# Kernel tuning notes

Hardware: AMD Instinct MI355X
Metric: run time of the kernel (lower is better)

## Reference

```python
import jax, jax.numpy as jnp
import numpy as np

B, S, D = 2, 2048, 1024
H, HD, R = 16, 64, 128
BLOCK, TOPK = 64, 4
ROPE_BASE = 100000.0
NEG = -1e30  # finite large-negative instead of -inf to avoid NaN rows


def _rope_tables(seq_len, dim, dtype):
    inv_freq = 1.0 / (ROPE_BASE ** (jnp.arange(0, dim, 2, dtype=jnp.float32) / dim))
    freqs = jnp.arange(seq_len, dtype=jnp.float32)[:, None] * inv_freq[None, :]  # [S, dim/2]
    emb = jnp.concatenate([freqs, freqs], axis=-1)  # [S, dim]
    return jnp.cos(emb).astype(dtype), jnp.sin(emb).astype(dtype)


def _rotate_half(t):
    t1, t2 = jnp.split(t, 2, axis=-1)
    return jnp.concatenate([-t2, t1], axis=-1)


def _apply_rope(t, cos, sin):
    # t: [B, H, S, HD]; cos/sin: [S, HD]
    return t * cos[None, None] + _rotate_half(t) * sin[None, None]


def setup_inputs() -> dict:
    key = jax.random.key(0)
    ks = jax.random.split(key, 6)
    s = 0.02
    return {
        "x": jax.random.normal(ks[0], (B, S, D), jnp.float32),
        "w_q": jax.random.normal(ks[1], (D, D), jnp.float32) * s,
        "w_kv_down": jax.random.normal(ks[2], (R, D), jnp.float32) * s,
        "w_kv_up": jax.random.normal(ks[3], (2 * D, R), jnp.float32) * s,
        "w_out": jax.random.normal(ks[4], (D, D), jnp.float32) * s,
        "w_scorer": jax.random.normal(ks[5], (1, D), jnp.float32) * s,
    }


def reference(x, w_q, w_kv_down, w_kv_up, w_out, w_scorer):
    b, s, d = x.shape
    nb = s // BLOCK  # S divisible by block_size here

    q = (x @ w_q.T).reshape(b, s, H, HD).transpose(0, 2, 1, 3)  # [B,H,S,HD]
    latent = x @ w_kv_down.T                                      # [B,S,R]
    kv = latent @ w_kv_up.T                                       # [B,S,2D]
    k, v = jnp.split(kv, 2, axis=-1)
    k = k.reshape(b, s, H, HD).transpose(0, 2, 1, 3)
    v = v.reshape(b, s, H, HD).transpose(0, 2, 1, 3)

    cos, sin = _rope_tables(s, HD, x.dtype)
    q = _apply_rope(q, cos, sin)
    k = _apply_rope(k, cos, sin)

    # block relevance scores from mean-pooled block reps of x
    block_reps = x.reshape(b, nb, BLOCK, d).mean(axis=2)          # [B,nb,D]
    block_scores = (block_reps @ w_scorer.T)[..., 0]              # [B,nb]
    _, top_idx = jax.lax.top_k(block_scores, min(TOPK, nb))       # [B,topk]

    # sparse key mask: True where key position lies in a selected block
    sel = jnp.zeros((b, nb), dtype=bool)
    sel = sel.at[jnp.arange(b)[:, None], top_idx].set(True)       # [B,nb]
    sparse_mask = jnp.repeat(sel, BLOCK, axis=1)                  # [B,S]

    causal = jnp.tril(jnp.ones((s, s), dtype=bool))               # True = allowed
    allowed = sparse_mask[:, None, None, :] & causal[None, None]  # [B,1,S,S]

    scale = 1.0 / jnp.sqrt(jnp.asarray(HD, x.dtype))
    scores = jnp.einsum("bhqd,bhkd->bhqk", q, k) * scale          # [B,H,S,S]
    scores = jnp.where(allowed, scores, NEG)
    attn = jax.nn.softmax(scores, axis=-1)
    out = jnp.einsum("bhqk,bhkd->bhqd", attn, v)                  # [B,H,S,HD]
    out = out.transpose(0, 2, 1, 3).reshape(b, s, d)
    return out @ w_out.T
```

## Files before the change

kernel.cpp:

```cpp
#include <hip/hip_runtime.h>
#include <hip/hip_bf16.h>
#include <math.h>

#define B_ 2
#define S_ 2048
#define D_ 1024
#define H_ 16
#define HD_ 64
#define R_ 128
#define NBLK 32
#define TOPK_ 4
#define BS_ (B_*S_)

typedef __attribute__((ext_vector_type(8))) short bf16x8;
typedef __attribute__((ext_vector_type(4))) float f32x4;

__device__ __forceinline__ unsigned short f2bf(float f) {
    unsigned int u = __float_as_uint(f);
    u += 0x7fffu + ((u >> 16) & 1u);
    return (unsigned short)(u >> 16);
}
__device__ __forceinline__ float bf2f(unsigned short h) {
    return __uint_as_float(((unsigned int)h) << 16);
}
__device__ __forceinline__ unsigned int pack2(float a, float b) {
    return (unsigned int)f2bf(a) | ((unsigned int)f2bf(b) << 16);
}
__device__ __forceinline__ void gload_lds16(const void* g, void* l) {
    __builtin_amdgcn_global_load_lds((const __attribute__((address_space(1))) void*)g,
                                     (__attribute__((address_space(3))) void*)l, 16, 0, 0);
}

__global__ void rope_tables_k(float* __restrict__ cosT, float* __restrict__ sinT) {
    int idx = blockIdx.x*256 + threadIdx.x;
    if (idx >= S_*HD_) return;
    int s  = idx >> 6;
    int hd = idx & 63;
    int j = (hd < 32) ? hd : hd - 32;
    float inv = powf(100000.0f, -((float)(2*j) / 64.0f));
    float fr = (float)s * inv;
    cosT[idx] = cosf(fr);
    sinT[idx] = sinf(fr);
}

__global__ __launch_bounds__(256) void cvtw_k(const float* __restrict__ wq,
        const float* __restrict__ wkd, const float* __restrict__ wku,
        const float* __restrict__ wo, unsigned short* __restrict__ wcat,
        unsigned short* __restrict__ wkub, unsigned short* __restrict__ wob) {
    const int blk = blockIdx.x;
    const float* src; unsigned short* dst; int base;
    if      (blk < 512) { src = wq;  dst = wcat;            base = blk;       }
    else if (blk < 576) { src = wkd; dst = wcat + 1048576;  base = blk - 512; }
    else if (blk < 704) { src = wku; dst = wkub;            base = blk - 576; }
    else                { src = wo;  dst = wob;             base = blk - 704; }
    const int i = base*2048 + threadIdx.x*8;
    float4 a = *(const float4*)&src[i];
    float4 b = *(const float4*)&src[i+4];
    uint4 o;
    o.x = pack2(a.x, a.y); o.y = pack2(a.z, a.w);
    o.z = pack2(b.x, b.y); o.w = pack2(b.z, b.w);
    *(uint4*)&dst[i] = o;
}

template<int EPI>
__global__ __launch_bounds__(256) void gemm_mfma_k(const unsigned short* __restrict__ A,
        const unsigned short* __restrict__ Bm, int M, int N, int K,
        void* __restrict__ o0, void* __restrict__ o1,
        const float* __restrict__ cosT, const float* __restrict__ sinT) {
    __shared__ unsigned short As[128*64];
    __shared__ unsigned short Bs[64*64];
    const int tid  = threadIdx.x;
    const int wave = tid >> 6, lane = tid & 63;
    const int bm = blockIdx.y << 7, bn = blockIdx.x << 6;
    const int g  = lane >> 4, qc = lane & 15;
    const int srow  = lane >> 3;
    const int sslot = (lane & 7) ^ srow;

    f32x4 acc[2][4];
    #pragma unroll
    for (int m=0;m<2;m++)
        #pragma unroll
        for (int n=0;n<4;n++)
            acc[m][n] = (f32x4){0.f,0.f,0.f,0.f};

    for (int k0 = 0; k0 < K; k0 += 64) {
        __syncthreads();
        #pragma unroll
        for (int it = 0; it < 4; ++it) {
            const int chunk = (it << 2) | wave;
            const int row   = (chunk << 3) | srow;
            gload_lds16(A + (size_t)(bm + row) * K + k0 + (sslot << 3), &As[chunk << 9]);
        }
        #pragma unroll
        for (int it = 0; it < 2; ++it) {
            const int chunk = (it << 2) | wave;
            const int row   = (chunk << 3) | srow;
            gload_lds16(Bm + (size_t)(bn + row) * K + k0 + (sslot << 3), &Bs[chunk << 9]);
        }
        __syncthreads();
        #pragma unroll
        for (int ks = 0; ks < 2; ++ks) {
            const int swb = ((ks << 2) | g) ^ (lane & 7);
            bf16x8 af[2], bfr[4];
            #pragma unroll
            for (int m = 0; m < 2; ++m)
                af[m]  = *(const bf16x8*)&As[(((wave << 5) + (m << 4) + qc) << 6) + (swb << 3)];
            #pragma unroll
            for (int n = 0; n < 4; ++n)
                bfr[n] = *(const bf16x8*)&Bs[(((n << 4) + qc) << 6) + (swb << 3)];
            #pragma unroll
            for (int m = 0; m < 2; ++m)
                #pragma unroll
                for (int n = 0; n < 4; ++n)
                    acc[m][n] = __builtin_amdgcn_mfma_f32_16x16x32_bf16(af[m], bfr[n], acc[m][n], 0, 0, 0);
        }
    }

    if (EPI == 0) {
        float* C = (float*)o0;
        #pragma unroll
        for (int m = 0; m < 2; ++m) {
            const int r0 = bm + (wave << 5) + (m << 4) + (g << 2);
            #pragma unroll
            for (int n = 0; n < 4; ++n) {
                const int c = bn + (n << 4) + qc;
                #pragma unroll
                for (int j = 0; j < 4; ++j)
                    C[(size_t)(r0 + j) * N + c] = acc[m][n][j];
            }
        }
    } else {
        const bool isrope = (bn < 1024);
        if (isrope) {
            const int h = bn >> 6;
            unsigned short* dst = (unsigned short*)o0;
            #pragma unroll
            for (int m = 0; m < 2; ++m) {
                const int r0 = bm + (wave << 5) + (m << 4) + (g << 2);
                #pragma unroll
                for (int j = 0; j < 4; ++j) {
                    const int row = r0 + j;
                    const int b = row >> 11, s = row & (S_-1);
                    const size_t obase = ((size_t)(b*H_ + h) * S_ + s) << 6;
                    #pragma unroll
                    for (int n = 0; n < 4; ++n) {
                        const int hd = (n << 4) + qc;
                        const float c_ = cosT[(s << 6) + hd];
                        const float sn = sinT[(s << 6) + hd];
                        const float rot = (n < 2) ? -acc[m][n ^ 2][j] : acc[m][n ^ 2][j];
                        dst[obase + hd] = f2bf(acc[m][n][j] * c_ + rot * sn);
                    }
                }
            }
        } else if (EPI == 1) {
            unsigned short* latb = (unsigned short*)o1;
            const int c0 = bn - 1024;
            #pragma unroll
            for (int m = 0; m < 2; ++m) {
                const int r0 = bm + (wave << 5) + (m << 4) + (g << 2);
                #pragma unroll
                for (int n = 0; n < 4; ++n) {
                    const int c = c0 + (n << 4) + qc;
                    #pragma unroll
                    for (int j = 0; j < 4; ++j)
                        latb[(size_t)(r0 + j) * R_ + c] = f2bf(acc[m][n][j]);
                }
            }
        } else {
            const int h = (bn >> 6) - 16;
            unsigned short* vrb = (unsigned short*)o1;
            #pragma unroll
            for (int m = 0; m < 2; ++m) {
                const int r0 = bm + (wave << 5) + (m << 4) + (g << 2);
                #pragma unroll
                for (int j = 0; j < 4; ++j) {
                    const int row = r0 + j;
                    const int b = row >> 11, s = row & (S_-1);
                    const size_t obase = ((size_t)(b*H_ + h) * S_ + s) << 6;
                    #pragma unroll
                    for (int n = 0; n < 4; ++n)
                        vrb[obase + (n << 4) + qc] = f2bf(acc[m][n][j]);
                }
            }
        }
    }
}

__global__ __launch_bounds__(256) void rowscore_cvt_k(const float* __restrict__ x,
        const float* __restrict__ wsc, float* __restrict__ rows,
        unsigned short* __restrict__ xb) {
    const int wid  = (blockIdx.x << 2) + (threadIdx.x >> 6);
    const int lane = threadIdx.x & 63;
    #pragma unroll
    for (int r = 0; r < 4; ++r) {
        const int row = (wid << 2) + r;
        const float* xp = x + (size_t)row * D_;
        unsigned short* xo = xb + (size_t)row * D_;
        float acc = 0.f;
        #pragma unroll
        for (int j = 0; j < 4; ++j) {
            const int off = ((j << 6) + lane) << 2;
            float4 xv = *(const float4*)&xp[off];
            float4 wv = *(const float4*)&wsc[off];
            acc = fmaf(xv.x, wv.x, acc);
            acc = fmaf(xv.y, wv.y, acc);
            acc = fmaf(xv.z, wv.z, acc);
            acc = fmaf(xv.w, wv.w, acc);
            uint2 o; o.x = pack2(xv.x, xv.y); o.y = pack2(xv.z, xv.w);
            *(uint2*)&xo[off] = o;
        }
        #pragma unroll
        for (int m = 1; m <= 32; m <<= 1) acc += __shfl_xor(acc, m);
        if (lane == 0) rows[row] = acc;
    }
}

__global__ __launch_bounds__(256) void blocktopk_k(const float* __restrict__ rows,
        int* __restrict__ sel) {
    __shared__ float bs[64];
    const int bk = threadIdx.x >> 2, qt = threadIdx.x & 3;
    const float* rp = rows + (bk << 6) + (qt << 4);
    float p = 0.f;
    #pragma unroll
    for (int i = 0; i < 16; ++i) p += rp[i];
    p += __shfl_xor(p, 1);
    p += __shfl_xor(p, 2);
    if (qt == 0) bs[bk] = p;
    __syncthreads();
    if (threadIdx.x < B_) {
        const int b = threadIdx.x;
        float sc[NBLK];
        for (int i = 0; i < NBLK; ++i) sc[i] = bs[b * NBLK + i];
        for (int j = 0; j < TOPK_; ++j) {
            float best = -INFINITY; int bi = 0;
            for (int i = 0; i < NBLK; ++i)
                if (sc[i] > best) { best = sc[i]; bi = i; }
            sel[b * TOPK_ + j] = bi;
            sc[bi] = -INFINITY;
        }
    }
}

__global__ __launch_bounds__(256) void vt_k(const unsigned short* __restrict__ vrb,
        unsigned short* __restrict__ vtb, float* __restrict__ vsum) {
    const int wg = blockIdx.x;
    const int bh = wg >> 5;
    __shared__ unsigned short T[64][72];
    const uint4* src = (const uint4*)(vrb + (size_t)wg*4096);
    #pragma unroll
    for (int u=0;u<2;u++) {
        int idx = (u<<8) + threadIdx.x;
        int r = idx>>3, c = (idx&7)<<3;
        *(uint4*)&T[r][c] = src[idx];
    }
    __syncthreads();
    unsigned short* dst = vtb + (size_t)wg*4096;
    #pragma unroll
    for (int u=0;u<2;u++) {
        int idx = (u<<8) + threadIdx.x;
        int dd = idx>>3, k0 = (idx&7)<<3;
        unsigned short tmp[8];
        float sm = 0.f;
        #pragma unroll
        for (int j=0;j<8;j++) { tmp[j] = T[k0+j][dd]; sm += bf2f(tmp[j]); }
        *(uint4*)&dst[(size_t)idx<<3] = *(uint4*)tmp;
        sm += __shfl_xor(sm, 1);
        sm += __shfl_xor(sm, 2);
        sm += __shfl_xor(sm, 4);
        if ((threadIdx.x & 7) == 0) atomicAdd(&vsum[(bh<<6)+dd], sm);
    }
}

__global__ __launch_bounds__(256) void attn_mfma_k(const unsigned short* __restrict__ qrb,
        const unsigned short* __restrict__ krb, const unsigned short* __restrict__ vtb,
        const int* __restrict__ sel, const float* __restrict__ vsum,
        unsigned short* __restrict__ attno) {
    const int qb = blockIdx.x & (NBLK-1);
    const int bh = blockIdx.x >> 5;
    const int b  = bh >> 4;
    const int h  = bh & 15;
    const int tid  = threadIdx.x;
    const int wave = tid >> 6, lane = tid & 63;
    const int g = lane >> 4, qc = lane & 15;

    __shared__ unsigned short Ks[64][72];
    __shared__ unsigned short Vt[64][72];
    __shared__ unsigned short Pl[4][16][72];
    __shared__ float cfl[4][16];
    __shared__ float lvl[4][16];

    int selb[4];
    #pragma unroll
    for (int j=0;j<4;j++) selb[j] = sel[(b<<2)+j];
    const bool diag = (selb[0]==qb)|(selb[1]==qb)|(selb[2]==qb)|(selb[3]==qb);

    const unsigned short* qp = qrb + (((size_t)bh*S_ + (qb<<6) + (wave<<4) + qc) << 6);
    bf16x8 bq[2];
    bq[0] = *(const bf16x8*)(qp + (g<<3));
    bq[1] = *(const bf16x8*)(qp + 32 + (g<<3));

    f32x4 oacc[4];
    #pragma unroll
    for (int n=0;n<4;n++) oacc[n] = (f32x4){0.f,0.f,0.f,0.f};
    float mrun = -INFINITY, lrun = 0.f;
    int nproc = 0;
    const int qib = (wave<<4) + qc;

    for (int j = 0; j < 5; ++j) {
        int kb; bool isdiag;
        if (j < 4) { kb = selb[j]; isdiag = false; if (kb >= qb) continue; }
        else       { if (!diag) continue; kb = qb; isdiag = true; }
        nproc++;
        const uint4* gk = (const uint4*)(krb + (((size_t)bh*S_ + (kb<<6)) << 6));
        const uint4* gv = (const uint4*)(vtb + (((size_t)(bh*NBLK + kb)) << 12));
        __syncthreads();
        #pragma unroll
        for (int u=0;u<2;u++) {
            int idx = (u<<8) + tid;
            int r = idx>>3, c = (idx&7)<<3;
            *(uint4*)&Ks[r][c] = gk[idx];
            *(uint4*)&Vt[r][c] = gv[idx];
        }
        __syncthreads();

        f32x4 sf[4];
        #pragma unroll
        for (int m=0;m<4;m++) sf[m] = (f32x4){0.f,0.f,0.f,0.f};
        #pragma unroll
        for (int ks=0;ks<2;ks++)
            #pragma unroll
            for (int m=0;m<4;m++) {
                bf16x8 ak = *(const bf16x8*)&Ks[(m<<4)+qc][(ks<<5)+(g<<3)];
                sf[m] = __builtin_amdgcn_mfma_f32_16x16x32_bf16(ak, bq[ks], sf[m], 0, 0, 0);
            }

        float s[16];
        float bmax = -INFINITY;
        #pragma unroll
        for (int m=0;m<4;m++)
            #pragma unroll
            for (int r2=0;r2<4;r2++) {
                const int kl = (m<<4)+(g<<2)+r2;
                float v = sf[m][r2]*0.125f;
                if (isdiag && kl > qib) v = -1e30f;
                s[(m<<2)+r2] = v;
                bmax = fmaxf(bmax, v);
            }
        bmax = fmaxf(bmax, __shfl_xor(bmax, 16));
        bmax = fmaxf(bmax, __shfl_xor(bmax, 32));
        const float mnew = fmaxf(mrun, bmax);
        const float cf = __expf(mrun - mnew);
        float ls = 0.f;
        #pragma unroll
        for (int m=0;m<4;m++) {
            float p0 = __expf(s[(m<<2)+0]-mnew);
            float p1 = __expf(s[(m<<2)+1]-mnew);
            float p2 = __expf(s[(m<<2)+2]-mnew);
            float p3 = __expf(s[(m<<2)+3]-mnew);
            ls += p0+p1+p2+p3;
            const int koff = (m<<4)+(g<<2);
            *(unsigned int*)&Pl[wave][qc][koff]   = pack2(p0,p1);
            *(unsigned int*)&Pl[wave][qc][koff+2] = pack2(p2,p3);
        }
        ls += __shfl_xor(ls, 16);
        ls += __shfl_xor(ls, 32);
        lrun = lrun*cf + ls;
        cfl[wave][qc] = cf;
        f32x4 cf4 = *(const f32x4*)&cfl[wave][g<<2];
        #pragma unroll
        for (int n=0;n<4;n++) oacc[n] *= cf4;
        #pragma unroll
        for (int ks=0;ks<2;ks++) {
            bf16x8 pa = *(const bf16x8*)&Pl[wave][qc][(ks<<5)+(g<<3)];
            #pragma unroll
            for (int n=0;n<4;n++) {
                bf16x8 vb = *(const bf16x8*)&Vt[(n<<4)+qc][(ks<<5)+(g<<3)];
                oacc[n] = __builtin_amdgcn_mfma_f32_16x16x32_bf16(pa, vb, oacc[n], 0, 0, 0);
            }
        }
        mrun = mnew;
    }

    f32x4 il4 = (f32x4){0.f,0.f,0.f,0.f};
    if (nproc) {
        lvl[wave][qc] = 1.0f / lrun;
        il4 = *(const f32x4*)&lvl[wave][g<<2];
    }
    #pragma unroll
    for (int n=0;n<4;n++)
        #pragma unroll
        for (int r2=0;r2<4;r2++) {
            float val = nproc ? oacc[n][r2]*il4[r2]
                              : vsum[(bh<<6)+(n<<4)+qc] * (1.0f/(float)S_);
            const int row = (qb<<6) + (wave<<4) + (g<<2) + r2;
            attno[(((size_t)(b*S_+row))<<10) + (h<<6) + (n<<4) + qc] = f2bf(val);
        }
}

extern "C" void kernel_launch(void* const* d_in, const int* in_sizes, int n_in,
                              void* d_out, int out_size, void* d_ws, size_t ws_size,
                              hipStream_t stream) {
    (void)in_sizes; (void)n_in; (void)out_size; (void)ws_size;
    const float* x     = (const float*)d_in[0];
    const float* w_q   = (const float*)d_in[1];
    const float* w_kvd = (const float*)d_in[2];
    const float* w_kvu = (const float*)d_in[3];
    const float* w_o   = (const float*)d_in[4];
    const float* w_sc  = (const float*)d_in[5];
    float* out = (float*)d_out;

    char* p = (char*)d_ws;
    auto alloc = [&](size_t bytes) -> void* {
        void* r = (void*)p;
        p += (bytes + 255) & ~(size_t)255;
        return r;
    };
    float* cosT  = (float*)alloc((size_t)S_*HD_*4);
    float* sinT  = (float*)alloc((size_t)S_*HD_*4);
    unsigned short* xb    = (unsigned short*)alloc((size_t)BS_*D_*2);
    unsigned short* wcat  = (unsigned short*)alloc((size_t)(D_+R_)*D_*2);
    unsigned short* wkub  = (unsigned short*)alloc((size_t)2*D_*R_*2);
    unsigned short* wob   = (unsigned short*)alloc((size_t)D_*D_*2);
    unsigned short* latb  = (unsigned short*)alloc((size_t)BS_*R_*2);
    unsigned short* qrb   = (unsigned short*)alloc((size_t)BS_*D_*2);
    unsigned short* krb   = (unsigned short*)alloc((size_t)BS_*D_*2);
    unsigned short* vrb   = (unsigned short*)alloc((size_t)BS_*D_*2);
    unsigned short* vtb   = (unsigned short*)alloc((size_t)BS_*D_*2);
    unsigned short* attnob= (unsigned short*)alloc((size_t)BS_*D_*2);
    float* rows   = (float*)alloc((size_t)BS_*4);
    int*   sel    = (int*)  alloc((size_t)B_*TOPK_*4);
    float* vsum   = (float*)alloc((size_t)B_*H_*HD_*4);

    rope_tables_k<<<(S_*HD_+255)/256, 256, 0, stream>>>(cosT, sinT);
    cvtw_k<<<1216, 256, 0, stream>>>(w_q, w_kvd, w_kvu, w_o, wcat, wkub, wob);
    rowscore_cvt_k<<<256, 256, 0, stream>>>(x, w_sc, rows, xb);
    blocktopk_k<<<1, 256, 0, stream>>>(rows, sel);

    gemm_mfma_k<1><<<dim3((D_+R_)/64, BS_/128), 256, 0, stream>>>(
        xb, wcat, BS_, D_+R_, D_, qrb, latb, cosT, sinT);
    gemm_mfma_k<2><<<dim3(2*D_/64, BS_/128), 256, 0, stream>>>(
        latb, wkub, BS_, 2*D_, R_, krb, vrb, cosT, sinT);

    hipMemsetAsync(vsum, 0, (size_t)B_*H_*HD_*4, stream);
    vt_k<<<B_*H_*NBLK, 256, 0, stream>>>(vrb, vtb, vsum);
    attn_mfma_k<<<B_*H_*NBLK, 256, 0, stream>>>(qrb, krb, vtb, sel, vsum, attnob);
    gemm_mfma_k<0><<<dim3(D_/64, BS_/128), 256, 0, stream>>>(
        attnob, wob, BS_, D_, D_, out, nullptr, nullptr, nullptr);
}
```

Measured before the change: 160.2 us.

## Fuse V transpose and column sums into KV-up GEMM epilogue; load K/V fragments directly

The separate vt_k kernel is removed. The KV-up GEMM epilogue now stages each V tile in shared memory, writes it out transposed per 64-key block, and atomically accumulates the per-head V column sums. This removes one launch and a full round trip of the intermediate V buffer through global memory. Separately, the attention kernel drops its shared-memory K/V staging and the two barriers per block, loading MFMA fragments straight from global memory into registers. That trades LDS traffic and synchronisation for uncoalesced global loads and higher register pressure.

```diff
diff --git a/kernel.cpp b/kernel.cpp
--- a/kernel.cpp
+++ b/kernel.cpp
@@ -66,9 +66,11 @@
 __global__ __launch_bounds__(256) void gemm_mfma_k(const unsigned short* __restrict__ A,
         const unsigned short* __restrict__ Bm, int M, int N, int K,
         void* __restrict__ o0, void* __restrict__ o1,
-        const float* __restrict__ cosT, const float* __restrict__ sinT) {
-    __shared__ unsigned short As[128*64];
-    __shared__ unsigned short Bs[64*64];
+        const float* __restrict__ cosT, const float* __restrict__ sinT,
+        float* __restrict__ vsum) {
+    __shared__ unsigned short shbuf[128*64 + 64*64];
+    unsigned short* As = shbuf;
+    unsigned short* Bs = shbuf + 128*64;
     const int tid  = threadIdx.x;
     const int wave = tid >> 6, lane = tid & 63;
     const int bm = blockIdx.y << 7, bn = blockIdx.x << 6;
@@ -167,19 +169,39 @@
                 }
             }
         } else {
-            const int h = (bn >> 6) - 16;
-            unsigned short* vrb = (unsigned short*)o1;
+            const int h  = (bn >> 6) - 16;
+            const int b  = bm >> 11, s0 = bm & (S_-1);
+            const int bh = (b << 4) + h;
+            unsigned short* vtb = (unsigned short*)o1;
+            unsigned short (*T)[72] = (unsigned short(*)[72])shbuf;
+            __syncthreads();
             #pragma unroll
             for (int m = 0; m < 2; ++m) {
-                const int r0 = bm + (wave << 5) + (m << 4) + (g << 2);
-                #pragma unroll
-                for (int j = 0; j < 4; ++j) {
-                    const int row = r0 + j;
-                    const int b = row >> 11, s = row & (S_-1);
-                    const size_t obase = ((size_t)(b*H_ + h) * S_ + s) << 6;
+                const int r0 = (wave << 5) + (m << 4) + (g << 2);
+                #pragma unroll
+                for (int n = 0; n < 4; ++n)
                     #pragma unroll
-                    for (int n = 0; n < 4; ++n)
-                        vrb[obase + (n << 4) + qc] = f2bf(acc[m][n][j]);
+                    for (int j = 0; j < 4; ++j)
+                        T[r0 + j][(n << 4) + qc] = f2bf(acc[m][n][j]);
+            }
+            __syncthreads();
+            #pragma unroll
+            for (int u = 0; u < 2; ++u) {
+                const int kb = (s0 >> 6) + u;
+                unsigned short* dst = vtb + (((size_t)(bh * NBLK + kb)) << 12);
+                #pragma unroll
+                for (int uu = 0; uu < 2; ++uu) {
+                    const int idx = (uu << 8) + tid;
+                    const int dd = idx >> 3, k0 = (idx & 7) << 3;
+                    unsigned short tmp[8];
+                    float sm = 0.f;
+                    #pragma unroll
+                    for (int j = 0; j < 8; ++j) { tmp[j] = T[(u << 6) + k0 + j][dd]; sm += bf2f(tmp[j]); }
+                    *(uint4*)&dst[(size_t)(dd << 6) + k0] = *(uint4*)tmp;
+                    sm += __shfl_xor(sm, 1);
+                    sm += __shfl_xor(sm, 2);
+                    sm += __shfl_xor(sm, 4);
+                    if ((tid & 7) == 0) atomicAdd(&vsum[(bh << 6) + dd], sm);
                 }
             }
         }
@@ -241,36 +263,6 @@
     }
 }
 
-__global__ __launch_bounds__(256) void vt_k(const unsigned short* __restrict__ vrb,
-        unsigned short* __restrict__ vtb, float* __restrict__ vsum) {
-    const int wg = blockIdx.x;
-    const int bh = wg >> 5;
-    __shared__ unsigned short T[64][72];
-    const uint4* src = (const uint4*)(vrb + (size_t)wg*4096);
-    #pragma unroll
-    for (int u=0;u<2;u++) {
-        int idx = (u<<8) + threadIdx.x;
-        int r = idx>>3, c = (idx&7)<<3;
-        *(uint4*)&T[r][c] = src[idx];
-    }
-    __syncthreads();
-    unsigned short* dst = vtb + (size_t)wg*4096;
-    #pragma unroll
-    for (int u=0;u<2;u++) {
-        int idx = (u<<8) + threadIdx.x;
-        int dd = idx>>3, k0 = (idx&7)<<3;
-        unsigned short tmp[8];
-        float sm = 0.f;
-        #pragma unroll
-        for (int j=0;j<8;j++) { tmp[j] = T[k0+j][dd]; sm += bf2f(tmp[j]); }
-        *(uint4*)&dst[(size_t)idx<<3] = *(uint4*)tmp;
-        sm += __shfl_xor(sm, 1);
-        sm += __shfl_xor(sm, 2);
-        sm += __shfl_xor(sm, 4);
-        if ((threadIdx.x & 7) == 0) atomicAdd(&vsum[(bh<<6)+dd], sm);
-    }
-}
-
 __global__ __launch_bounds__(256) void attn_mfma_k(const unsigned short* __restrict__ qrb,
         const unsigned short* __restrict__ krb, const unsigned short* __restrict__ vtb,
         const int* __restrict__ sel, const float* __restrict__ vsum,
@@ -283,8 +275,6 @@
     const int wave = tid >> 6, lane = tid & 63;
     const int g = lane >> 4, qc = lane & 15;
 
-    __shared__ unsigned short Ks[64][72];
-    __shared__ unsigned short Vt[64][72];
     __shared__ unsigned short Pl[4][16][72];
     __shared__ float cfl[4][16];
     __shared__ float lvl[4][16];
@@ -311,17 +301,20 @@
         if (j < 4) { kb = selb[j]; isdiag = false; if (kb >= qb) continue; }
         else       { if (!diag) continue; kb = qb; isdiag = true; }
         nproc++;
-        const uint4* gk = (const uint4*)(krb + (((size_t)bh*S_ + (kb<<6)) << 6));
-        const uint4* gv = (const uint4*)(vtb + (((size_t)(bh*NBLK + kb)) << 12));
-        __syncthreads();
-        #pragma unroll
-        for (int u=0;u<2;u++) {
-            int idx = (u<<8) + tid;
-            int r = idx>>3, c = (idx&7)<<3;
-            *(uint4*)&Ks[r][c] = gk[idx];
-            *(uint4*)&Vt[r][c] = gv[idx];
-        }
-        __syncthreads();
+        const unsigned short* kB = krb + (((size_t)bh*S_ + (kb<<6)) << 6);
+        const unsigned short* vT = vtb + (((size_t)(bh*NBLK + kb)) << 12);
+
+        bf16x8 ak[2][4], vb[2][4];
+        #pragma unroll
+        for (int ks=0;ks<2;ks++)
+            #pragma unroll
+            for (int m=0;m<4;m++)
+                ak[ks][m] = *(const bf16x8*)(kB + (((m<<4)+qc)<<6) + (ks<<5) + (g<<3));
+        #pragma unroll
+        for (int ks=0;ks<2;ks++)
+            #pragma unroll
+            for (int n=0;n<4;n++)
+                vb[ks][n] = *(const bf16x8*)(vT + (((n<<4)+qc)<<6) + (ks<<5) + (g<<3));
 
         f32x4 sf[4];
         #pragma unroll
@@ -329,10 +322,8 @@
         #pragma unroll
         for (int ks=0;ks<2;ks++)
             #pragma unroll
-            for (int m=0;m<4;m++) {
-                bf16x8 ak = *(const bf16x8*)&Ks[(m<<4)+qc][(ks<<5)+(g<<3)];
-                sf[m] = __builtin_amdgcn_mfma_f32_16x16x32_bf16(ak, bq[ks], sf[m], 0, 0, 0);
-            }
+            for (int m=0;m<4;m++)
+                sf[m] = __builtin_amdgcn_mfma_f32_16x16x32_bf16(ak[ks][m], bq[ks], sf[m], 0, 0, 0);
 
         float s[16];
         float bmax = -INFINITY;
@@ -373,10 +364,8 @@
         for (int ks=0;ks<2;ks++) {
             bf16x8 pa = *(const bf16x8*)&Pl[wave][qc][(ks<<5)+(g<<3)];
             #pragma unroll
-            for (int n=0;n<4;n++) {
-                bf16x8 vb = *(const bf16x8*)&Vt[(n<<4)+qc][(ks<<5)+(g<<3)];
-                oacc[n] = __builtin_amdgcn_mfma_f32_16x16x32_bf16(pa, vb, oacc[n], 0, 0, 0);
-            }
+            for (int n=0;n<4;n++)
+                oacc[n] = __builtin_amdgcn_mfma_f32_16x16x32_bf16(pa, vb[ks][n], oacc[n], 0, 0, 0);
         }
         mrun = mnew;
     }
@@ -424,7 +413,6 @@
     unsigned short* latb  = (unsigned short*)alloc((size_t)BS_*R_*2);
     unsigned short* qrb   = (unsigned short*)alloc((size_t)BS_*D_*2);
     unsigned short* krb   = (unsigned short*)alloc((size_t)BS_*D_*2);
-    unsigned short* vrb   = (unsigned short*)alloc((size_t)BS_*D_*2);
     unsigned short* vtb   = (unsigned short*)alloc((size_t)BS_*D_*2);
     unsigned short* attnob= (unsigned short*)alloc((size_t)BS_*D_*2);
     float* rows   = (float*)alloc((size_t)BS_*4);
@@ -437,13 +425,12 @@
     blocktopk_k<<<1, 256, 0, stream>>>(rows, sel);
 
     gemm_mfma_k<1><<<dim3((D_+R_)/64, BS_/128), 256, 0, stream>>>(
-        xb, wcat, BS_, D_+R_, D_, qrb, latb, cosT, sinT);
+        xb, wcat, BS_, D_+R_, D_, qrb, latb, cosT, sinT, nullptr);
+    hipMemsetAsync(vsum, 0, (size_t)B_*H_*HD_*4, stream);
     gemm_mfma_k<2><<<dim3(2*D_/64, BS_/128), 256, 0, stream>>>(
-        latb, wkub, BS_, 2*D_, R_, krb, vrb, cosT, sinT);
-
-    hipMemsetAsync(vsum, 0, (size_t)B_*H_*HD_*4, stream);
-    vt_k<<<B_*H_*NBLK, 256, 0, stream>>>(vrb, vtb, vsum);
+        latb, wkub, BS_, 2*D_, R_, krb, vtb, cosT, sinT, vsum);
+
     attn_mfma_k<<<B_*H_*NBLK, 256, 0, stream>>>(qrb, krb, vtb, sel, vsum, attnob);
     gemm_mfma_k<0><<<dim3(D_/64, BS_/128), 256, 0, stream>>>(
-        attnob, wob, BS_, D_, D_, out, nullptr, nullptr, nullptr);
-}
+        attnob, wob, BS_, D_, D_, out, nullptr, nullptr, nullptr, nullptr);
+}
```

Result: slower. 169.3 us (+5.7%).
